# Kernel optimization log

Measured on AMD Instinct MI355X. Metric: run time of the kernel, lower is better.

The kernel has to match this reference:

```python
import jax, jax.numpy as jnp
import numpy as np

B, T, E, H = 8, 2048, 128, 4
FACTOR = 3  # autocorr_factor


def setup_inputs() -> dict:
    key = jax.random.key(0)
    ks = jax.random.split(key, 9)
    s = 0.05
    return {
        "hidden_states": jax.random.normal(ks[0], (B, T, E), jnp.float32),
        "wq": jax.random.normal(ks[1], (E, E, H), jnp.float32) * s,
        "bq": jax.random.normal(ks[2], (E, H), jnp.float32) * s,
        "wk": jax.random.normal(ks[3], (E, E, H), jnp.float32) * s,
        "bk": jax.random.normal(ks[4], (E, H), jnp.float32) * s,
        "wv": jax.random.normal(ks[5], (E, E, H), jnp.float32) * s,
        "bv": jax.random.normal(ks[6], (E, H), jnp.float32) * s,
        "wo": jax.random.normal(ks[7], (E, H, E), jnp.float32) * s,
        "bo": jax.random.normal(ks[8], (E,), jnp.float32) * s,
    }


def reference(hidden_states, wq, bq, wk, bk, wv, bv, wo, bo):
    # Inference path (training=None) of AutoCorrelation.call
    bsize, seq_len, _ = hidden_states.shape
    q = jnp.einsum('btj,juh->btuh', hidden_states, wq) + bq  # [B,T,E,H]
    k = jnp.einsum('btj,juh->btuh', hidden_states, wk) + bk
    v = jnp.einsum('btj,juh->btuh', hidden_states, wv) + bv

    # FFT cross-correlation over time axis
    qf = jnp.fft.rfft(q.transpose(0, 2, 3, 1), n=seq_len, axis=-1)  # [B,E,H,F]
    kf = jnp.fft.rfft(k.transpose(0, 2, 3, 1), n=seq_len, axis=-1)
    ac = jnp.fft.irfft(qf * jnp.conj(kf), n=seq_len, axis=-1)       # [B,E,H,T]
    ac = ac.transpose(0, 3, 1, 2)                                   # [B,T,E,H]

    ac_mean = ac.mean(axis=-1)                                      # [B,T,E]
    top_k = int(FACTOR * np.log(float(seq_len)))

    # top-k delays per (batch, channel)
    vals, idx = jax.lax.top_k(ac_mean.transpose(0, 2, 1), top_k)    # [B,E,K]
    w = jax.nn.softmax(vals, axis=-1)  # == Softmax(axis=-2) on [B,K,E]

    # NOTE: in the source, `delays_agg +=` is dedented outside the top_k loop,
    # so only the LAST iteration (i = top_k-1) contributes. Replicated faithfully.
    delay = idx[:, :, top_k - 1]   # [B,E] int
    wgt = w[:, :, top_k - 1]       # [B,E]

    # gather over doubled values == circular roll by -delay per (b, channel)
    t_idx = (jnp.arange(seq_len)[None, :, None] + delay[:, None, :]) % seq_len  # [B,T,E]
    rolled = jnp.take_along_axis(v, t_idx[..., None], axis=1)       # [B,T,E,H]
    agg = rolled * wgt[:, None, :, None]                            # [B,T,E,H]

    return jnp.einsum('btjh,jhf->btf', agg, wo) + bo                # [B,T,E]
```

## Files before the change

kernel.cpp:

```cpp
#include <hip/hip_runtime.h>
#include <math.h>

#define TSEQ 2048
#define BB 8
#define EE 128
#define HH 4
#define UHN 512
#define KTOP 22
#define BT (BB*TSEQ)
#define APITCH 40
#define OPITCH 76

typedef _Float16 f16;
typedef f16 f16x2 __attribute__((ext_vector_type(2)));
typedef f16 f16x4 __attribute__((ext_vector_type(4)));
typedef f16 f16x8 __attribute__((ext_vector_type(8)));
typedef float f32x4 __attribute__((ext_vector_type(4)));
typedef float cpx  __attribute__((ext_vector_type(2)));

__device__ __forceinline__ cpx cmul(cpx a, cpx b) {
  cpx r = (cpx){a.x, a.x} * b;
  r += (cpx){-a.y, a.y} * (cpx){b.y, b.x};
  return r;
}
template<int SGN>
__device__ __forceinline__ cpx muli(cpx b) {
  return (SGN < 0) ? (cpx){b.y, -b.x} : (cpx){-b.y, b.x};
}

__device__ __forceinline__ f16x8 ld_frag(const f16* p) {
  f16x4 lo = *(const f16x4*)(p);
  f16x4 hi = *(const f16x4*)(p + 16);
  return __builtin_shufflevector(lo, hi, 0, 1, 2, 3, 4, 5, 6, 7);
}

__global__ __launch_bounds__(256)
void prep_kernel(const float* __restrict__ hs,
                 const float* __restrict__ wq, const float* __restrict__ wk,
                 const float* __restrict__ wv, const float* __restrict__ wo,
                 f16* __restrict__ hs_h, f16* __restrict__ hs_l,
                 f16* __restrict__ Wt_h, f16* __restrict__ Wt_l,
                 f16* __restrict__ wo_t)
{
  __shared__ float tile[64][65];
  const int bx = blockIdx.x, tid = threadIdx.x;

  if (bx < 1024) {
    size_t base = ((size_t)bx*256 + tid) * 8;
    float4 a = *(const float4*)&hs[base];
    float4 b = *(const float4*)&hs[base + 4];
    float vf[8] = {a.x,a.y,a.z,a.w, b.x,b.y,b.z,b.w};
    f16 h[8], l[8];
#pragma unroll
    for (int j = 0; j < 8; ++j) { h[j] = (f16)vf[j]; l[j] = (f16)(vf[j] - (float)h[j]); }
    *(f16x8*)&hs_h[base] = (f16x8){h[0],h[1],h[2],h[3],h[4],h[5],h[6],h[7]};
    *(f16x8*)&hs_l[base] = (f16x8){l[0],l[1],l[2],l[3],l[4],l[5],l[6],l[7]};
  } else if (bx < 1072) {
    int r = bx - 1024;
    int z = r >> 4, rem = r & 15, kt = rem & 1, uht = rem >> 1;
    const float* W = (z == 0) ? wq : (z == 1) ? wk : wv;
#pragma unroll
    for (int rr = 0; rr < 16; ++rr) {
      int idx = tid + 256*rr;
      int krow = idx >> 6, ucol = idx & 63;
      tile[krow][ucol] = W[(size_t)(kt*64 + krow)*UHN + uht*64 + ucol];
    }
    __syncthreads();
#pragma unroll
    for (int rr = 0; rr < 16; ++rr) {
      int idx = tid + 256*rr;
      int orow = idx >> 6, ocol = idx & 63;
      float w = tile[ocol][orow];
      f16 h = (f16)w;
      size_t o = ((size_t)z*UHN + uht*64 + orow)*EE + kt*64 + ocol;
      Wt_h[o] = h;
      Wt_l[o] = (f16)(w - (float)h);
    }
  } else {
    int r = bx - 1072;
    int ft = r & 1, uht = r >> 1;
#pragma unroll
    for (int rr = 0; rr < 16; ++rr) {
      int idx = tid + 256*rr;
      int urow = idx >> 6, fcol = idx & 63;
      tile[urow][fcol] = wo[(size_t)(uht*64 + urow)*EE + ft*64 + fcol];
    }
    __syncthreads();
#pragma unroll
    for (int rr = 0; rr < 16; ++rr) {
      int idx = tid + 256*rr;
      int orow = idx >> 6, ocol = idx & 63;
      wo_t[(size_t)(ft*64 + orow)*UHN + uht*64 + ocol] = (f16)tile[ocol][orow];
    }
  }
}

__global__ __launch_bounds__(256, 3)
void proj_mfma(const f16* __restrict__ hs_h, const f16* __restrict__ hs_l,
               const f16* __restrict__ Wt_h, const f16* __restrict__ Wt_l,
               const float* __restrict__ bq, const float* __restrict__ bk,
               const float* __restrict__ bv,
               float* __restrict__ q_t, float* __restrict__ k_t, f16* __restrict__ v_t)
{
  __shared__ f16 Ah[128*APITCH];
  __shared__ f16 Al[128*APITCH];
  __shared__ f16 Bh[128*APITCH];
  __shared__ f16 Bl[128*APITCH];

  const int z = blockIdx.z;
  const float* bias = (z == 0) ? bq : (z == 1) ? bk : bv;
  const f16* WH = Wt_h + (size_t)z*UHN*EE;
  const f16* WL = Wt_l + (size_t)z*UHN*EE;

  const int tid  = threadIdx.x;
  const int lane = tid & 63, wid = tid >> 6;
  const int wm = wid >> 1, wn = wid & 1;
  const int ln15 = lane & 15, g = lane >> 4;
  const int uh0 = blockIdx.x * 128;
  const int bt0 = blockIdx.y * 128;

  f32x4 acc[4][4] = {};

  for (int kc = 0; kc < 4; ++kc) {
    const int k0 = kc * 32;
    __syncthreads();
#pragma unroll
    for (int r = 0; r < 2; ++r) {
      int idx = tid + 256*r;
      int row = idx >> 2, seg = (idx & 3) << 3;
      size_t ga = (size_t)(uh0 + row)*EE + k0 + seg;
      *(f16x8*)&Ah[row*APITCH + seg] = *(const f16x8*)&WH[ga];
      *(f16x8*)&Al[row*APITCH + seg] = *(const f16x8*)&WL[ga];
      size_t gb = (size_t)(bt0 + row)*EE + k0 + seg;
      *(f16x8*)&Bh[row*APITCH + seg] = *(const f16x8*)&hs_h[gb];
      *(f16x8*)&Bl[row*APITCH + seg] = *(const f16x8*)&hs_l[gb];
    }
    __syncthreads();
    const int kb = 4*g;
    f16x8 a_h[4], a_l[4], b_h[4], b_l[4];
#pragma unroll
    for (int mf = 0; mf < 4; ++mf) {
      int off = (wm*64 + mf*16 + ln15)*APITCH + kb;
      a_h[mf] = ld_frag(&Ah[off]);
      a_l[mf] = ld_frag(&Al[off]);
    }
#pragma unroll
    for (int nf = 0; nf < 4; ++nf) {
      int off = (wn*64 + nf*16 + ln15)*APITCH + kb;
      b_h[nf] = ld_frag(&Bh[off]);
      b_l[nf] = ld_frag(&Bl[off]);
    }
#pragma unroll
    for (int mf = 0; mf < 4; ++mf)
#pragma unroll
      for (int nf = 0; nf < 4; ++nf) {
        acc[mf][nf] = __builtin_amdgcn_mfma_f32_16x16x32_f16(a_h[mf], b_h[nf], acc[mf][nf], 0, 0, 0);
        acc[mf][nf] = __builtin_amdgcn_mfma_f32_16x16x32_f16(a_h[mf], b_l[nf], acc[mf][nf], 0, 0, 0);
        acc[mf][nf] = __builtin_amdgcn_mfma_f32_16x16x32_f16(a_l[mf], b_h[nf], acc[mf][nf], 0, 0, 0);
      }
  }

  const int b = bt0 >> 11, tb = bt0 & (TSEQ - 1);
  if (z == 2) {
#pragma unroll
    for (int mf = 0; mf < 4; ++mf) {
      int uhb = uh0 + wm*64 + mf*16 + g*4;
      f32x4 bias4 = *(const f32x4*)&bias[uhb];
#pragma unroll
      for (int r = 0; r < 4; ++r) {
        f16* vrow = v_t + ((size_t)(b*UHN + uhb + r))*TSEQ + tb;
#pragma unroll
        for (int nf = 0; nf < 4; ++nf)
          vrow[wn*64 + nf*16 + ln15] = (f16)(acc[mf][nf][r] + bias4[r]);
      }
    }
  } else {
    float* outp = (z == 0) ? q_t : k_t;
#pragma unroll
    for (int mf = 0; mf < 4; ++mf) {
      int uhb = uh0 + wm*64 + mf*16 + g*4;
      f32x4 bias4 = *(const f32x4*)&bias[uhb];
#pragma unroll
      for (int r = 0; r < 4; ++r) {
        size_t rowbase = ((size_t)(b*UHN + uhb + r))*TSEQ + tb;
#pragma unroll
        for (int nf = 0; nf < 4; ++nf)
          outp[rowbase + wn*64 + nf*16 + ln15] = acc[mf][nf][r] + bias4[r];
      }
    }
  }
}

#define ZPAD(g) ((g) + ((g) >> 5))

template<int SGN>
__device__ __forceinline__ void dft8(const cpx* u, cpx* y) {
  const float r2 = 0.70710678118654752440f;
  cpx a0 = u[0] + u[4], a1 = u[1] + u[5];
  cpx a2 = u[2] + u[6], a3 = u[3] + u[7];
  cpx b0 = u[0] - u[4], b1 = u[1] - u[5];
  cpx b2 = u[2] - u[6], b3 = u[3] - u[7];
  cpx t1 = (b1 + muli<SGN>(b1)) * r2;
  cpx t2 = muli<SGN>(b2);
  cpx e  = (b3 + muli<SGN>(b3)) * r2;
  cpx t3 = muli<SGN>(e);
  {
    cpx c0 = a0 + a2, c1 = a0 - a2;
    cpx c2 = a1 + a3, c3 = a1 - a3;
    y[0] = c0 + c2; y[4] = c0 - c2;
    y[2] = c1 + muli<SGN>(c3); y[6] = c1 - muli<SGN>(c3);
  }
  {
    cpx c0 = b0 + t2, c1 = b0 - t2;
    cpx c2 = t1 + t3, c3 = t1 - t3;
    y[1] = c0 + c2; y[5] = c0 - c2;
    y[3] = c1 + muli<SGN>(c3); y[7] = c1 - muli<SGN>(c3);
  }
}

__device__ __forceinline__ void wpow_tree(cpx w1, cpx* W) {
  W[0] = w1;
  cpx w2 = cmul(w1, w1);
  cpx w4 = cmul(w2, w2);
  W[1] = w2;
  W[2] = cmul(w2, w1);
  W[3] = w4;
  W[4] = cmul(w4, w1);
  W[5] = cmul(w4, w2);
  W[6] = cmul(w4, W[2]);
}

__device__ __forceinline__ void fwd_radix8(cpx* Z, cpx w1, int base, int eighth) {
  cpx u[8];
#pragma unroll
  for (int t = 0; t < 8; ++t) u[t] = Z[ZPAD(base + eighth*t)];
  cpx y[8];
  dft8<-1>(u, y);
  cpx W[7];
  wpow_tree(w1, W);
  Z[ZPAD(base)] = y[0];
#pragma unroll
  for (int s = 1; s < 8; ++s)
    Z[ZPAD(base + eighth*s)] = cmul(y[s], W[s-1]);
}

__device__ __forceinline__ void inv_radix8(cpx* Z, cpx w1c, int base, int eighth) {
  cpx u[8];
#pragma unroll
  for (int t = 0; t < 8; ++t) u[t] = Z[ZPAD(base + eighth*t)];
  cpx W[7];
  wpow_tree(w1c, W);
#pragma unroll
  for (int t = 1; t < 8; ++t) u[t] = cmul(u[t], W[t-1]);
  cpx y[8];
  dft8<1>(u, y);
#pragma unroll
  for (int s = 0; s < 8; ++s) Z[ZPAD(base + eighth*s)] = y[s];
}

template<int SGN>
__device__ __forceinline__ void radix4_stage(cpx* Z, int base) {
  cpx v0 = Z[ZPAD(base)], v1 = Z[ZPAD(base+1)];
  cpx v2 = Z[ZPAD(base+2)], v3 = Z[ZPAD(base+3)];
  cpx c0 = v0 + v2, c1 = v0 - v2;
  cpx c2 = v1 + v3, c3 = v1 - v3;
  Z[ZPAD(base)]   = c0 + c2;
  Z[ZPAD(base+1)] = c1 + muli<SGN>(c3);
  Z[ZPAD(base+2)] = c0 - c2;
  Z[ZPAD(base+3)] = c1 - muli<SGN>(c3);
}

__global__ __launch_bounds__(256)
void fftcorr_topk(const float* __restrict__ q_t, const float* __restrict__ k_t,
                  int* __restrict__ delay, float* __restrict__ wgt)
{
  __shared__ cpx Z[2112];
  __shared__ cpx twl[292];

  const int tid = threadIdx.x;
  const int bu  = blockIdx.x;

  for (int idx = tid; idx < 292; idx += 256) {
    float ang;
    if (idx < 256)      ang = -6.2831853071795864769f * (float)idx / 2048.0f;
    else if (idx < 288) ang = -6.2831853071795864769f * (float)(idx - 256) / 256.0f;
    else                ang = -6.2831853071795864769f * (float)(idx - 288) / 32.0f;
    float s, c;
    sincosf(ang, &s, &c);
    twl[idx] = (cpx){c, s};
  }
  const cpx* tw1 = twl;
  const cpx* tw2 = twl + 256;
  const cpx* tw3 = twl + 288;

  int pp[8];
#pragma unroll
  for (int r = 0; r < 8; ++r) {
    int p = tid + (r << 8);
    int f = ((p >> 8) & 7) | (((p >> 5) & 7) << 3) | (((p >> 2) & 7) << 6) | ((p & 3) << 9);
    int nf = (2048 - f) & 2047;
    pp[r] = ((nf & 7) << 8) | (((nf >> 3) & 7) << 5) | (((nf >> 6) & 7) << 2) | ((nf >> 9) & 3);
  }
  cpx sreg[8] = {};
  __syncthreads();

  for (int h = 0; h < HH; ++h) {
    const float* qp = q_t + ((size_t)bu*HH + h)*TSEQ;
    const float* kp = k_t + ((size_t)bu*HH + h)*TSEQ;
    if (h) __syncthreads();
    {
      cpx u[8];
#pragma unroll
      for (int t = 0; t < 8; ++t)
        u[t] = (cpx){qp[tid + 256*t], kp[tid + 256*t]};
      cpx y[8];
      dft8<-1>(u, y);
      cpx W[7];
      wpow_tree(tw1[tid], W);
      Z[ZPAD(tid)] = y[0];
#pragma unroll
      for (int s = 1; s < 8; ++s)
        Z[ZPAD(tid + 256*s)] = cmul(y[s], W[s-1]);
    }
    __syncthreads();
    fwd_radix8(Z, tw2[tid & 31], ((tid >> 5) << 8) + (tid & 31), 32);
    __syncthreads();
    fwd_radix8(Z, tw3[tid & 3], ((tid >> 2) << 5) + (tid & 3), 4);
    __syncthreads();
    radix4_stage<-1>(Z, 4*tid);
    radix4_stage<-1>(Z, 4*(tid + 256));
    __syncthreads();
#pragma unroll
    for (int r = 0; r < 8; ++r) {
      int p = tid + (r << 8);
      cpx A  = Z[ZPAD(p)];
      cpx Zp = Z[ZPAD(pp[r])];
      sreg[r].x += 0.5f  * (Zp.x*A.y + Zp.y*A.x);
      sreg[r].y += 0.25f * ((A.x*A.x + A.y*A.y) - (Zp.x*Zp.x + Zp.y*Zp.y));
    }
  }
  __syncthreads();

#pragma unroll
  for (int r = 0; r < 8; ++r) Z[ZPAD(tid + (r << 8))] = sreg[r];
  __syncthreads();
  radix4_stage<1>(Z, 4*tid);
  radix4_stage<1>(Z, 4*(tid + 256));
  __syncthreads();
  { cpx w = tw3[tid & 3]; w.y = -w.y;
    inv_radix8(Z, w, ((tid >> 2) << 5) + (tid & 3), 4); }
  __syncthreads();
  { cpx w = tw2[tid & 31]; w.y = -w.y;
    inv_radix8(Z, w, ((tid >> 5) << 8) + (tid & 31), 32); }
  __syncthreads();

  float* vbuf = (float*)Z;
  float* lmf  = vbuf + 2048;
  int*   lii  = (int*)(vbuf + 2304);
  {
    cpx u[8];
#pragma unroll
    for (int t = 0; t < 8; ++t) u[t] = Z[ZPAD(tid + 256*t)];
    __syncthreads();
    cpx w1c = tw1[tid]; w1c.y = -w1c.y;
    cpx W[7];
    wpow_tree(w1c, W);
#pragma unroll
    for (int t = 1; t < 8; ++t) u[t] = cmul(u[t], W[t-1]);
    cpx y[8];
    dft8<1>(u, y);
    const float scale = 1.0f / (float)(TSEQ * HH);
    float lb = -3.4e38f; int lbi = tid;
#pragma unroll
    for (int s = 0; s < 8; ++s) {
      float x = y[s].x * scale;
      vbuf[tid + 256*s] = x;
      if (x > lb) { lb = x; lbi = tid + 256*s; }
    }
    lmf[tid] = lb;
    lii[tid] = lbi;
  }
  __syncthreads();

  if (tid < 64) {
    const int lane = tid;
    float m0 = 0.f, ssum = 0.f;
    for (int it = 0; it < KTOP; ++it) {
      float best = -3.4e38f; int bi = 0x40000000;
#pragma unroll
      for (int e = 0; e < 4; ++e) {
        float x = lmf[4*lane + e];
        int  xi = lii[4*lane + e];
        if (x > best || (x == best && xi < bi)) { best = x; bi = xi; }
      }
#pragma unroll
      for (int off = 32; off > 0; off >>= 1) {
        float ob = __shfl_down(best, off);
        int   oi = __shfl_down(bi, off);
        if (ob > best || (ob == best && oi < bi)) { best = ob; bi = oi; }
      }
      float gb = __shfl(best, 0);
      int   gi = __shfl(bi, 0);
      int   ow = gi & 255;
      if (lane == (ow >> 2)) {
        vbuf[gi] = -3.4e38f;
        float nb = -3.4e38f; int ni = ow;
#pragma unroll
        for (int s = 0; s < 8; ++s) {
          float x = vbuf[ow + 256*s];
          if (x > nb) { nb = x; ni = ow + 256*s; }
        }
        lmf[ow] = nb;
        lii[ow] = ni;
      }
      if (lane == 0) {
        if (it == 0) m0 = gb;
        ssum += expf(gb - m0);
        if (it == KTOP - 1) {
          delay[bu] = gi;
          wgt[bu]   = expf(gb - m0) / ssum;
        }
      }
    }
  }
}

__global__ __launch_bounds__(256)
void out_mfma(const f16* __restrict__ v_t, const int* __restrict__ delay,
              const float* __restrict__ wgt, const f16* __restrict__ wo_t,
              const float* __restrict__ bo, float* __restrict__ out)
{
  __shared__ f16 Af[64*OPITCH];
  __shared__ f16 Bf[64*OPITCH];
  __shared__ int   dly[EE];
  __shared__ float wg[EE];

  const int tid  = threadIdx.x;
  const int lane = tid & 63, wid = tid >> 6;
  const int wm = wid >> 1, wn = wid & 1;
  const int ln15 = lane & 15, g = lane >> 4;
  const int t0g = blockIdx.x * 64;
  const int f0  = blockIdx.y * 64;
  const int b = t0g >> 11, t0 = t0g & (TSEQ - 1);

  if (tid < EE) { dly[tid] = delay[b*EE + tid]; wg[tid] = wgt[b*EE + tid]; }

  f32x4 acc[2][2] = {};

  for (int c = 0; c < 8; ++c) {
    const int uh0 = c * 64;
    __syncthreads();
#pragma unroll
    for (int r = 0; r < 16; ++r) {
      int idx = tid + 256*r;
      int tl = idx & 63, ul = idx >> 6;
      int u = (uh0 + ul) >> 2;
      float x = (float)v_t[((size_t)(b*UHN + uh0 + ul))*TSEQ + ((t0 + tl + dly[u]) & (TSEQ-1))]
                * wg[u];
      Af[tl*OPITCH + ul] = (f16)x;
    }
#pragma unroll
    for (int r = 0; r < 2; ++r) {
      int idx = tid + 256*r;
      int fl = idx >> 3, seg = (idx & 7) << 3;
      const f16* src = &wo_t[(size_t)(f0 + fl)*UHN + uh0 + seg];
      *(f16x4*)&Bf[fl*OPITCH + seg]     = *(const f16x4*)(src);
      *(f16x4*)&Bf[fl*OPITCH + seg + 4] = *(const f16x4*)(src + 4);
    }
    __syncthreads();
#pragma unroll
    for (int ks = 0; ks < 2; ++ks) {
      const int kb = ks*32 + 4*g;
      f16x8 av[2], bv[2];
#pragma unroll
      for (int mf = 0; mf < 2; ++mf)
        av[mf] = ld_frag(&Af[(wm*32 + mf*16 + ln15)*OPITCH + kb]);
#pragma unroll
      for (int nf = 0; nf < 2; ++nf)
        bv[nf] = ld_frag(&Bf[(wn*32 + nf*16 + ln15)*OPITCH + kb]);
#pragma unroll
      for (int mf = 0; mf < 2; ++mf)
#pragma unroll
        for (int nf = 0; nf < 2; ++nf)
          acc[mf][nf] = __builtin_amdgcn_mfma_f32_16x16x32_f16(av[mf], bv[nf], acc[mf][nf], 0, 0, 0);
    }
  }

#pragma unroll
  for (int mf = 0; mf < 2; ++mf)
#pragma unroll
    for (int r = 0; r < 4; ++r) {
      int bt = t0g + wm*32 + mf*16 + g*4 + r;
#pragma unroll
      for (int nf = 0; nf < 2; ++nf) {
        int f = f0 + wn*32 + nf*16 + ln15;
        out[(size_t)bt*EE + f] = acc[mf][nf][r] + bo[f];
      }
    }
}

extern "C" void kernel_launch(void* const* d_in, const int* in_sizes, int n_in,
                              void* d_out, int out_size, void* d_ws, size_t ws_size,
                              hipStream_t stream) {
  (void)in_sizes; (void)n_in; (void)out_size; (void)ws_size;
  const float* hs = (const float*)d_in[0];
  const float* wq = (const float*)d_in[1];
  const float* bq = (const float*)d_in[2];
  const float* wk = (const float*)d_in[3];
  const float* bk = (const float*)d_in[4];
  const float* wv = (const float*)d_in[5];
  const float* bv = (const float*)d_in[6];
  const float* wo = (const float*)d_in[7];
  const float* bo = (const float*)d_in[8];
  float* out = (float*)d_out;

  char* p = (char*)d_ws;
  float* q_t  = (float*)p;  p += (size_t)BB*UHN*TSEQ*4;
  float* k_t  = (float*)p;  p += (size_t)BB*UHN*TSEQ*4;
  f16*   v_t  = (f16*)p;    p += (size_t)BB*UHN*TSEQ*2;
  f16*   hs_h = (f16*)p;    p += (size_t)BT*EE*2;
  f16*   hs_l = (f16*)p;    p += (size_t)BT*EE*2;
  f16*   Wt_h = (f16*)p;    p += (size_t)3*UHN*EE*2;
  f16*   Wt_l = (f16*)p;    p += (size_t)3*UHN*EE*2;
  f16*   wo_t = (f16*)p;    p += (size_t)EE*UHN*2;
  int*   delay = (int*)p;   p += BB*EE*4;
  float* wgt   = (float*)p;

  prep_kernel<<<dim3(1088), 256, 0, stream>>>(hs, wq, wk, wv, wo,
                                              hs_h, hs_l, Wt_h, Wt_l, wo_t);
  proj_mfma<<<dim3(4, 128, 3), 256, 0, stream>>>(hs_h, hs_l, Wt_h, Wt_l,
                                                 bq, bk, bv, q_t, k_t, v_t);
  fftcorr_topk<<<dim3(1024), 256, 0, stream>>>(q_t, k_t, delay, wgt);
  out_mfma<<<dim3(256, 2), 256, 0, stream>>>(v_t, delay, wgt, wo_t, bo, out);
}
```

Before: 116.1 us.

## Vectorize rolled-V gather, halve out tile, and swizzle projection block order

The output GEMM now gives each thread 8 contiguous time steps of one channel row, loaded with a single 16-byte read when the window does not wrap, instead of 16 scattered scalar gathers. Its tile shrinks to 32 time rows, which doubles the grid to 512x2 blocks for better occupancy. The projection kernel remaps its flat block index so that consecutively launched blocks spread across bt tiles in an XCD-aware pattern. The unaligned 16-byte memcpy may still be split into smaller loads, and each block now does less MFMA work to amortize its weight-tile loads.

```diff
diff --git a/kernel.cpp b/kernel.cpp
--- a/kernel.cpp
+++ b/kernel.cpp
@@ -116,8 +116,10 @@
   const int lane = tid & 63, wid = tid >> 6;
   const int wm = wid >> 1, wn = wid & 1;
   const int ln15 = lane & 15, g = lane >> 4;
-  const int uh0 = blockIdx.x * 128;
-  const int bt0 = blockIdx.y * 128;
+  const int fidx = blockIdx.y*4 + blockIdx.x;
+  const int work = (fidx & 7)*64 + (fidx >> 3);
+  const int uh0 = (work & 3) * 128;
+  const int bt0 = (work >> 2) * 128;
 
   f32x4 acc[4][4] = {};
 
@@ -430,7 +432,7 @@
               const float* __restrict__ wgt, const f16* __restrict__ wo_t,
               const float* __restrict__ bo, float* __restrict__ out)
 {
-  __shared__ f16 Af[64*OPITCH];
+  __shared__ f16 Af[32*OPITCH];
   __shared__ f16 Bf[64*OPITCH];
   __shared__ int   dly[EE];
   __shared__ float wg[EE];
@@ -439,25 +441,33 @@
   const int lane = tid & 63, wid = tid >> 6;
   const int wm = wid >> 1, wn = wid & 1;
   const int ln15 = lane & 15, g = lane >> 4;
-  const int t0g = blockIdx.x * 64;
+  const int t0g = blockIdx.x * 32;
   const int f0  = blockIdx.y * 64;
   const int b = t0g >> 11, t0 = t0g & (TSEQ - 1);
 
   if (tid < EE) { dly[tid] = delay[b*EE + tid]; wg[tid] = wgt[b*EE + tid]; }
 
-  f32x4 acc[2][2] = {};
+  f32x4 acc[2] = {};
 
   for (int c = 0; c < 8; ++c) {
     const int uh0 = c * 64;
     __syncthreads();
-#pragma unroll
-    for (int r = 0; r < 16; ++r) {
-      int idx = tid + 256*r;
-      int tl = idx & 63, ul = idx >> 6;
+    {
+      int ul = tid & 63, tg = tid >> 6;
       int u = (uh0 + ul) >> 2;
-      float x = (float)v_t[((size_t)(b*UHN + uh0 + ul))*TSEQ + ((t0 + tl + dly[u]) & (TSEQ-1))]
-                * wg[u];
-      Af[tl*OPITCH + ul] = (f16)x;
+      const f16* vrow = v_t + (size_t)(b*UHN + uh0 + ul)*TSEQ;
+      int st = (t0 + tg*8 + dly[u]) & (TSEQ - 1);
+      float wgu = wg[u];
+      f16 tmp[8];
+      if (st <= TSEQ - 8) {
+        __builtin_memcpy(tmp, vrow + st, 16);
+      } else {
+#pragma unroll
+        for (int j = 0; j < 8; ++j) tmp[j] = vrow[(st + j) & (TSEQ - 1)];
+      }
+#pragma unroll
+      for (int j = 0; j < 8; ++j)
+        Af[(tg*8 + j)*OPITCH + ul] = (f16)((float)tmp[j] * wgu);
     }
 #pragma unroll
     for (int r = 0; r < 2; ++r) {
@@ -471,32 +481,26 @@
 #pragma unroll
     for (int ks = 0; ks < 2; ++ks) {
       const int kb = ks*32 + 4*g;
-      f16x8 av[2], bv[2];
-#pragma unroll
-      for (int mf = 0; mf < 2; ++mf)
-        av[mf] = ld_frag(&Af[(wm*32 + mf*16 + ln15)*OPITCH + kb]);
+      f16x8 av = ld_frag(&Af[(wm*16 + ln15)*OPITCH + kb]);
+      f16x8 bv[2];
 #pragma unroll
       for (int nf = 0; nf < 2; ++nf)
         bv[nf] = ld_frag(&Bf[(wn*32 + nf*16 + ln15)*OPITCH + kb]);
 #pragma unroll
-      for (int mf = 0; mf < 2; ++mf)
-#pragma unroll
-        for (int nf = 0; nf < 2; ++nf)
-          acc[mf][nf] = __builtin_amdgcn_mfma_f32_16x16x32_f16(av[mf], bv[nf], acc[mf][nf], 0, 0, 0);
-    }
-  }
-
-#pragma unroll
-  for (int mf = 0; mf < 2; ++mf)
-#pragma unroll
-    for (int r = 0; r < 4; ++r) {
-      int bt = t0g + wm*32 + mf*16 + g*4 + r;
-#pragma unroll
-      for (int nf = 0; nf < 2; ++nf) {
-        int f = f0 + wn*32 + nf*16 + ln15;
-        out[(size_t)bt*EE + f] = acc[mf][nf][r] + bo[f];
-      }
-    }
+      for (int nf = 0; nf < 2; ++nf)
+        acc[nf] = __builtin_amdgcn_mfma_f32_16x16x32_f16(av, bv[nf], acc[nf], 0, 0, 0);
+    }
+  }
+
+#pragma unroll
+  for (int r = 0; r < 4; ++r) {
+    int bt = t0g + wm*16 + g*4 + r;
+#pragma unroll
+    for (int nf = 0; nf < 2; ++nf) {
+      int f = f0 + wn*32 + nf*16 + ln15;
+      out[(size_t)bt*EE + f] = acc[nf][r] + bo[f];
+    }
+  }
 }
 
 extern "C" void kernel_launch(void* const* d_in, const int* in_sizes, int n_in,
@@ -531,5 +535,5 @@
   proj_mfma<<<dim3(4, 128, 3), 256, 0, stream>>>(hs_h, hs_l, Wt_h, Wt_l,
                                                  bq, bk, bv, q_t, k_t, v_t);
   fftcorr_topk<<<dim3(1024), 256, 0, stream>>>(q_t, k_t, delay, wgt);
-  out_mfma<<<dim3(256, 2), 256, 0, stream>>>(v_t, delay, wgt, wo_t, bo, out);
-}
+  out_mfma<<<dim3(512, 2), 256, 0, stream>>>(v_t, delay, wgt, wo_t, bo, out);
+}
```

Result: no change. 117.4 us (+1.2%).

## Batch two heads per FFT pass and vectorize rolled V gather

Applied to the files above, without the earlier changes.

The FFT correlation kernel now transforms two heads at once, using a doubled shared-memory buffer. This halves the number of barrier-separated stage rounds and gives each thread more independent work to hide latency. The output GEMM's gather of the rolled V values now has each thread load 8 consecutive time steps with one 16-byte copy, with a scalar path for wraparound, instead of 16 scattered scalar loads per thread. The larger shared memory and register footprint may lower occupancy, and the 16-byte copy from an arbitrary offset may be unaligned.

```diff
diff --git a/kernel.cpp b/kernel.cpp
--- a/kernel.cpp
+++ b/kernel.cpp
@@ -230,18 +230,27 @@
   W[6] = cmul(w4, W[2]);
 }
 
-__device__ __forceinline__ void fwd_radix8(cpx* Z, cpx w1, int base, int eighth) {
-  cpx u[8];
-#pragma unroll
-  for (int t = 0; t < 8; ++t) u[t] = Z[ZPAD(base + eighth*t)];
-  cpx y[8];
-  dft8<-1>(u, y);
+__device__ __forceinline__ void fwd_radix8_x2(cpx* Z0, cpx* Z1, cpx w1,
+                                              int base, int eighth) {
+  cpx u0[8], u1[8];
+#pragma unroll
+  for (int t = 0; t < 8; ++t) {
+    u0[t] = Z0[ZPAD(base + eighth*t)];
+    u1[t] = Z1[ZPAD(base + eighth*t)];
+  }
   cpx W[7];
   wpow_tree(w1, W);
-  Z[ZPAD(base)] = y[0];
+  cpx y[8];
+  dft8<-1>(u0, y);
+  Z0[ZPAD(base)] = y[0];
 #pragma unroll
   for (int s = 1; s < 8; ++s)
-    Z[ZPAD(base + eighth*s)] = cmul(y[s], W[s-1]);
+    Z0[ZPAD(base + eighth*s)] = cmul(y[s], W[s-1]);
+  dft8<-1>(u1, y);
+  Z1[ZPAD(base)] = y[0];
+#pragma unroll
+  for (int s = 1; s < 8; ++s)
+    Z1[ZPAD(base + eighth*s)] = cmul(y[s], W[s-1]);
 }
 
 __device__ __forceinline__ void inv_radix8(cpx* Z, cpx w1c, int base, int eighth) {
@@ -274,11 +283,13 @@
 void fftcorr_topk(const float* __restrict__ q_t, const float* __restrict__ k_t,
                   int* __restrict__ delay, float* __restrict__ wgt)
 {
-  __shared__ cpx Z[2112];
+  __shared__ cpx Z[2*2112];
   __shared__ cpx twl[292];
 
   const int tid = threadIdx.x;
   const int bu  = blockIdx.x;
+  cpx* Z0 = Z;
+  cpx* Z1 = Z + 2112;
 
   for (int idx = tid; idx < 292; idx += 256) {
     float ang;
@@ -304,63 +315,78 @@
   cpx sreg[8] = {};
   __syncthreads();
 
-  for (int h = 0; h < HH; ++h) {
-    const float* qp = q_t + ((size_t)bu*HH + h)*TSEQ;
-    const float* kp = k_t + ((size_t)bu*HH + h)*TSEQ;
-    if (h) __syncthreads();
+  for (int hp = 0; hp < 2; ++hp) {
+    const float* qp0 = q_t + ((size_t)bu*HH + 2*hp    )*TSEQ;
+    const float* kp0 = k_t + ((size_t)bu*HH + 2*hp    )*TSEQ;
+    const float* qp1 = q_t + ((size_t)bu*HH + 2*hp + 1)*TSEQ;
+    const float* kp1 = k_t + ((size_t)bu*HH + 2*hp + 1)*TSEQ;
+    if (hp) __syncthreads();
     {
-      cpx u[8];
-#pragma unroll
-      for (int t = 0; t < 8; ++t)
-        u[t] = (cpx){qp[tid + 256*t], kp[tid + 256*t]};
-      cpx y[8];
-      dft8<-1>(u, y);
+      cpx u0[8], u1[8];
+#pragma unroll
+      for (int t = 0; t < 8; ++t) {
+        u0[t] = (cpx){qp0[tid + 256*t], kp0[tid + 256*t]};
+        u1[t] = (cpx){qp1[tid + 256*t], kp1[tid + 256*t]};
+      }
       cpx W[7];
       wpow_tree(tw1[tid], W);
-      Z[ZPAD(tid)] = y[0];
+      cpx y[8];
+      dft8<-1>(u0, y);
+      Z0[ZPAD(tid)] = y[0];
 #pragma unroll
       for (int s = 1; s < 8; ++s)
-        Z[ZPAD(tid + 256*s)] = cmul(y[s], W[s-1]);
-    }
-    __syncthreads();
-    fwd_radix8(Z, tw2[tid & 31], ((tid >> 5) << 8) + (tid & 31), 32);
-    __syncthreads();
-    fwd_radix8(Z, tw3[tid & 3], ((tid >> 2) << 5) + (tid & 3), 4);
-    __syncthreads();
-    radix4_stage<-1>(Z, 4*tid);
-    radix4_stage<-1>(Z, 4*(tid + 256));
+        Z0[ZPAD(tid + 256*s)] = cmul(y[s], W[s-1]);
+      dft8<-1>(u1, y);
+      Z1[ZPAD(tid)] = y[0];
+#pragma unroll
+      for (int s = 1; s < 8; ++s)
+        Z1[ZPAD(tid + 256*s)] = cmul(y[s], W[s-1]);
+    }
+    __syncthreads();
+    fwd_radix8_x2(Z0, Z1, tw2[tid & 31], ((tid >> 5) << 8) + (tid & 31), 32);
+    __syncthreads();
+    fwd_radix8_x2(Z0, Z1, tw3[tid & 3], ((tid >> 2) << 5) + (tid & 3), 4);
+    __syncthreads();
+    radix4_stage<-1>(Z0, 4*tid);
+    radix4_stage<-1>(Z0, 4*(tid + 256));
+    radix4_stage<-1>(Z1, 4*tid);
+    radix4_stage<-1>(Z1, 4*(tid + 256));
     __syncthreads();
 #pragma unroll
     for (int r = 0; r < 8; ++r) {
       int p = tid + (r << 8);
-      cpx A  = Z[ZPAD(p)];
-      cpx Zp = Z[ZPAD(pp[r])];
+      cpx A  = Z0[ZPAD(p)];
+      cpx Zp = Z0[ZPAD(pp[r])];
       sreg[r].x += 0.5f  * (Zp.x*A.y + Zp.y*A.x);
       sreg[r].y += 0.25f * ((A.x*A.x + A.y*A.y) - (Zp.x*Zp.x + Zp.y*Zp.y));
-    }
-  }
-  __syncthreads();
-
-#pragma unroll
-  for (int r = 0; r < 8; ++r) Z[ZPAD(tid + (r << 8))] = sreg[r];
-  __syncthreads();
-  radix4_stage<1>(Z, 4*tid);
-  radix4_stage<1>(Z, 4*(tid + 256));
+      A  = Z1[ZPAD(p)];
+      Zp = Z1[ZPAD(pp[r])];
+      sreg[r].x += 0.5f  * (Zp.x*A.y + Zp.y*A.x);
+      sreg[r].y += 0.25f * ((A.x*A.x + A.y*A.y) - (Zp.x*Zp.x + Zp.y*Zp.y));
+    }
+  }
+  __syncthreads();
+
+#pragma unroll
+  for (int r = 0; r < 8; ++r) Z0[ZPAD(tid + (r << 8))] = sreg[r];
+  __syncthreads();
+  radix4_stage<1>(Z0, 4*tid);
+  radix4_stage<1>(Z0, 4*(tid + 256));
   __syncthreads();
   { cpx w = tw3[tid & 3]; w.y = -w.y;
-    inv_radix8(Z, w, ((tid >> 2) << 5) + (tid & 3), 4); }
+    inv_radix8(Z0, w, ((tid >> 2) << 5) + (tid & 3), 4); }
   __syncthreads();
   { cpx w = tw2[tid & 31]; w.y = -w.y;
-    inv_radix8(Z, w, ((tid >> 5) << 8) + (tid & 31), 32); }
-  __syncthreads();
-
-  float* vbuf = (float*)Z;
+    inv_radix8(Z0, w, ((tid >> 5) << 8) + (tid & 31), 32); }
+  __syncthreads();
+
+  float* vbuf = (float*)Z0;
   float* lmf  = vbuf + 2048;
   int*   lii  = (int*)(vbuf + 2304);
   {
     cpx u[8];
 #pragma unroll
-    for (int t = 0; t < 8; ++t) u[t] = Z[ZPAD(tid + 256*t)];
+    for (int t = 0; t < 8; ++t) u[t] = Z0[ZPAD(tid + 256*t)];
     __syncthreads();
     cpx w1c = tw1[tid]; w1c.y = -w1c.y;
     cpx W[7];
@@ -451,13 +477,23 @@
     const int uh0 = c * 64;
     __syncthreads();
 #pragma unroll
-    for (int r = 0; r < 16; ++r) {
+    for (int r = 0; r < 2; ++r) {
       int idx = tid + 256*r;
-      int tl = idx & 63, ul = idx >> 6;
+      int ul = idx & 63, tg = idx >> 6;
       int u = (uh0 + ul) >> 2;
-      float x = (float)v_t[((size_t)(b*UHN + uh0 + ul))*TSEQ + ((t0 + tl + dly[u]) & (TSEQ-1))]
-                * wg[u];
-      Af[tl*OPITCH + ul] = (f16)x;
+      const f16* vrow = v_t + (size_t)(b*UHN + uh0 + ul)*TSEQ;
+      int st = (t0 + tg*8 + dly[u]) & (TSEQ - 1);
+      float wgu = wg[u];
+      f16 tmp[8];
+      if (st <= TSEQ - 8) {
+        __builtin_memcpy(tmp, vrow + st, 16);
+      } else {
+#pragma unroll
+        for (int j = 0; j < 8; ++j) tmp[j] = vrow[(st + j) & (TSEQ - 1)];
+      }
+#pragma unroll
+      for (int j = 0; j < 8; ++j)
+        Af[(tg*8 + j)*OPITCH + ul] = (f16)((float)tmp[j] * wgu);
     }
 #pragma unroll
     for (int r = 0; r < 2; ++r) {
```

Measured after the change: 123.0 us. 1.06x slower.

## Split FFT correlation into per-head-pair forward kernel and inverse top-k kernel

Applied to the files above, without the earlier changes.

The fused FFT-correlation kernel is split in two. The first kernel launches twice as many blocks, each handling two of the four heads, and writes a partial cross-spectrum to global memory. The second kernel sums the two partials and runs the inverse FFT and top-k. This aims to raise parallelism and latency hiding in the forward FFT, at the cost of an extra launch and a global write and read of the partial spectra. The partial buffer reuses the q_t workspace, which is safe only because each block overwrites just the q data it has already read.

```diff
diff --git a/kernel.cpp b/kernel.cpp
--- a/kernel.cpp
+++ b/kernel.cpp
@@ -271,14 +271,14 @@
 }
 
 __global__ __launch_bounds__(256)
-void fftcorr_topk(const float* __restrict__ q_t, const float* __restrict__ k_t,
-                  int* __restrict__ delay, float* __restrict__ wgt)
+void fft_fwd(const float* q_t, const float* k_t, cpx* Spart)
 {
   __shared__ cpx Z[2112];
   __shared__ cpx twl[292];
 
   const int tid = threadIdx.x;
-  const int bu  = blockIdx.x;
+  const int bu  = blockIdx.x >> 1;
+  const int hp  = blockIdx.x & 1;
 
   for (int idx = tid; idx < 292; idx += 256) {
     float ang;
@@ -304,10 +304,11 @@
   cpx sreg[8] = {};
   __syncthreads();
 
-  for (int h = 0; h < HH; ++h) {
+  for (int r2 = 0; r2 < 2; ++r2) {
+    const int h = 2*hp + r2;
     const float* qp = q_t + ((size_t)bu*HH + h)*TSEQ;
     const float* kp = k_t + ((size_t)bu*HH + h)*TSEQ;
-    if (h) __syncthreads();
+    if (r2) __syncthreads();
     {
       cpx u[8];
 #pragma unroll
@@ -338,6 +339,43 @@
       sreg[r].x += 0.5f  * (Zp.x*A.y + Zp.y*A.x);
       sreg[r].y += 0.25f * ((A.x*A.x + A.y*A.y) - (Zp.x*Zp.x + Zp.y*Zp.y));
     }
+  }
+
+  cpx* Sp = Spart + ((size_t)bu*2 + hp)*TSEQ;
+#pragma unroll
+  for (int r = 0; r < 8; ++r)
+    Sp[tid + (r << 8)] = sreg[r];
+}
+
+__global__ __launch_bounds__(256)
+void fft_inv_topk(const cpx* __restrict__ Spart, int* __restrict__ delay,
+                  float* __restrict__ wgt)
+{
+  __shared__ cpx Z[2112];
+  __shared__ cpx twl[292];
+
+  const int tid = threadIdx.x;
+  const int bu  = blockIdx.x;
+
+  for (int idx = tid; idx < 292; idx += 256) {
+    float ang;
+    if (idx < 256)      ang = -6.2831853071795864769f * (float)idx / 2048.0f;
+    else if (idx < 288) ang = -6.2831853071795864769f * (float)(idx - 256) / 256.0f;
+    else                ang = -6.2831853071795864769f * (float)(idx - 288) / 32.0f;
+    float s, c;
+    sincosf(ang, &s, &c);
+    twl[idx] = (cpx){c, s};
+  }
+  const cpx* tw1 = twl;
+  const cpx* tw2 = twl + 256;
+  const cpx* tw3 = twl + 288;
+
+  const cpx* S0 = Spart + (size_t)bu*2*TSEQ;
+  cpx sreg[8];
+#pragma unroll
+  for (int r = 0; r < 8; ++r) {
+    int p = tid + (r << 8);
+    sreg[r] = S0[p] + S0[TSEQ + p];
   }
   __syncthreads();
 
@@ -525,11 +563,13 @@
   f16*   wo_t = (f16*)p;    p += (size_t)EE*UHN*2;
   int*   delay = (int*)p;   p += BB*EE*4;
   float* wgt   = (float*)p;
+  cpx*   Spart = (cpx*)q_t;
 
   prep_kernel<<<dim3(1088), 256, 0, stream>>>(hs, wq, wk, wv, wo,
                                               hs_h, hs_l, Wt_h, Wt_l, wo_t);
   proj_mfma<<<dim3(4, 128, 3), 256, 0, stream>>>(hs_h, hs_l, Wt_h, Wt_l,
                                                  bq, bk, bv, q_t, k_t, v_t);
-  fftcorr_topk<<<dim3(1024), 256, 0, stream>>>(q_t, k_t, delay, wgt);
+  fft_fwd<<<dim3(2048), 256, 0, stream>>>(q_t, k_t, Spart);
+  fft_inv_topk<<<dim3(1024), 256, 0, stream>>>(Spart, delay, wgt);
   out_mfma<<<dim3(256, 2), 256, 0, stream>>>(v_t, delay, wgt, wo_t, bo, out);
 }
```

After: 120.4 us. 3.8% more time.
